# Kernel optimization log

Measured on AMD Instinct MI355X. Metric: run time of the kernel, lower is better.

Reference implementation:

```python
import jax, jax.numpy as jnp
import numpy as np

NUM_HEADS = 4
HEAD_DIM = 64
BN_EPS = 1e-5


def setup_inputs() -> dict:
    key = jax.random.key(0)
    ks = jax.random.split(key, 6)
    B, C, H, W = 8, 256, 48, 48
    HD = NUM_HEADS * HEAD_DIM  # 256
    x = jax.random.normal(ks[0], (B, C, H, W), dtype=jnp.float32)
    q_w = jax.random.normal(ks[1], (HD, C), dtype=jnp.float32) * (1.0 / np.sqrt(C))
    k_w = jax.random.normal(ks[2], (HEAD_DIM, C), dtype=jnp.float32) * (1.0 / np.sqrt(C))
    v_w = jax.random.normal(ks[3], (HEAD_DIM, C), dtype=jnp.float32) * (1.0 / np.sqrt(C))
    proj_w = jax.random.normal(ks[4], (C, HD), dtype=jnp.float32) * (1.0 / np.sqrt(HD))
    proj_b = jnp.zeros((C,), dtype=jnp.float32)
    gamma = jnp.ones((C,), dtype=jnp.float32)
    beta = jnp.zeros((C,), dtype=jnp.float32)
    return {"x": x, "q_w": q_w, "k_w": k_w, "v_w": v_w,
            "proj_w": proj_w, "proj_b": proj_b, "gamma": gamma, "beta": beta}


def reference(x, q_w, k_w, v_w, proj_w, proj_b, gamma, beta):
    B, C, H, W = x.shape
    N = H * W
    scale = HEAD_DIM ** -0.5
    xf = x.reshape(B, C, N)  # 1x1 conv == channel matmul
    q = jnp.einsum('oc,bcn->bon', q_w, xf).reshape(B, NUM_HEADS, HEAD_DIM, N)
    k = jnp.einsum('dc,bcn->bdn', k_w, xf)  # shared single KV head (MQA)
    v = jnp.einsum('dc,bcn->bdn', v_w, xf)
    # scores: [B, heads, N, N]
    attn = jnp.einsum('bhdn,bdm->bhnm', q, k) * scale
    attn = jax.nn.softmax(attn, axis=-1)
    out = jnp.einsum('bhnm,bdm->bhdn', attn, v)  # [B, heads, d, N]
    out = out.reshape(B, NUM_HEADS * HEAD_DIM, N)
    out = jnp.einsum('co,bon->bcn', proj_w, out) + proj_b[None, :, None]
    out = out.reshape(B, C, H, W)
    # BatchNorm2d (training-mode batch statistics, biased variance)
    mean = jnp.mean(out, axis=(0, 2, 3), keepdims=True)
    var = jnp.var(out, axis=(0, 2, 3), keepdims=True)
    out = gamma[None, :, None, None] * (out - mean) * jax.lax.rsqrt(var + BN_EPS) + beta[None, :, None, None]
    return out + x
```

## Files before the change

kernel.cpp:

```cpp
#include <hip/hip_runtime.h>
#include <hip/hip_bf16.h>
#include <math.h>

#define BB 8
#define CCH 256
#define NN 2304
#define NH 4
#define HDIM 64
#define QKV_ROWS 384
#define BN_EPS 1e-5f
#define NTILES 36
#define HTILES 18
#define SLOG2E 0.18033688011112042f

typedef short bf16x8 __attribute__((ext_vector_type(8)));
typedef short bf16x4 __attribute__((ext_vector_type(4)));
typedef float f32x4 __attribute__((ext_vector_type(4)));

#if __has_builtin(__builtin_amdgcn_exp2f)
#define EXP2(x) __builtin_amdgcn_exp2f(x)
#else
#define EXP2(x) __expf((x) * 0.6931471805599453f)
#endif

#define MFMA16(a, b, c) __builtin_amdgcn_mfma_f32_16x16x16bf16_1k(a, b, c, 0, 0, 0)
#define MFMA32(a, b, c) __builtin_amdgcn_mfma_f32_16x16x32_bf16(a, b, c, 0, 0, 0)

__device__ __forceinline__ unsigned bfpair(float a, float b) {
    __hip_bfloat162 h = __float22bfloat162_rn(make_float2(a, b));
    return *(unsigned*)&h;
}
__device__ __forceinline__ unsigned short f2bf(float f) {
    unsigned u = __float_as_uint(f);
    u = (u + 0x7FFFu + ((u >> 16) & 1u)) >> 16;
    return (unsigned short)u;
}
__device__ __forceinline__ bf16x4 pack4(float p0, float p1, float p2, float p3) {
    union { unsigned u[2]; bf16x4 v; } x;
    x.u[0] = bfpair(p0, p1);
    x.u[1] = bfpair(p2, p3);
    return x.v;
}
__device__ __forceinline__ float bf2f(unsigned short s) {
    return __uint_as_float((unsigned)s << 16);
}

__global__ __launch_bounds__(256) void cvt_x_k(
    const float* __restrict__ x, unsigned short* __restrict__ xT)
{
    __shared__ float sX[64][65];
    const int tid = threadIdx.x;
    const int b  = blockIdx.x;
    const int nb = blockIdx.y * 64;
    const int cb = blockIdx.z * 64;

    #pragma unroll
    for (int u = 0; u < 4; ++u) {
        int c  = (tid >> 4) + 16 * u;
        int n4 = (tid & 15) * 4;
        float4 v = *(const float4*)(x + ((size_t)(b * CCH + cb + c)) * NN + nb + n4);
        sX[c][n4+0] = v.x; sX[c][n4+1] = v.y; sX[c][n4+2] = v.z; sX[c][n4+3] = v.w;
    }
    __syncthreads();

    const int n  = tid >> 2;
    const int cg = (tid & 3) * 16;
    unsigned vals[8];
    #pragma unroll
    for (int p = 0; p < 8; ++p)
        vals[p] = bfpair(sX[cg + 2*p][n], sX[cg + 2*p + 1][n]);
    unsigned short* dst = xT + ((size_t)(b * NN + nb + n)) * CCH + cb + cg;
    *(uint4*)dst = make_uint4(vals[0], vals[1], vals[2], vals[3]);
    *(uint4*)(dst + 8) = make_uint4(vals[4], vals[5], vals[6], vals[7]);
}

__global__ __launch_bounds__(256) void cvt_w_k(
    const float* __restrict__ qw, const float* __restrict__ kw,
    const float* __restrict__ vw, const float* __restrict__ pw,
    unsigned short* __restrict__ Wb, unsigned short* __restrict__ Pb)
{
    int idx = blockIdx.x * 256 + threadIdx.x;
    if (idx < 98304) {
        int o = idx >> 8, c = idx & 255;
        float v;
        if (o < 256)      v = qw[(size_t)o * CCH + c] * SLOG2E;
        else if (o < 320) v = kw[(size_t)(o - 256) * CCH + c];
        else              v = vw[(size_t)(o - 320) * CCH + c];
        Wb[idx] = f2bf(v);
    } else {
        int j = idx - 98304;
        if (j < 65536) Pb[j] = f2bf(pw[j]);
    }
}

__global__ __launch_bounds__(128) void qkv_mfma_k(
    const unsigned short* __restrict__ Wb, const unsigned short* __restrict__ xT,
    unsigned short* __restrict__ Qt, unsigned short* __restrict__ Kt,
    unsigned short* __restrict__ Vn)
{
    __shared__ unsigned short sE[2][64 * 72];
    const int tid = threadIdx.x;
    const int wave = tid >> 6;
    const int lane = tid & 63;
    const int quad = lane >> 4;
    const int l15  = lane & 15;
    const int b  = blockIdx.x;
    const int nb = blockIdx.y * 64;
    const int mb = blockIdx.z * 128 + wave * 64;

    const unsigned short* Ab = Wb + (size_t)(mb + l15) * CCH + quad * 8;
    const unsigned short* Bb = xT + ((size_t)(b * NN + nb + l15)) * CCH + quad * 8;

    f32x4 C[4][4] = {};
    for (int k0 = 0; k0 < CCH; k0 += 32) {
        bf16x8 aA[4], bB[4];
        #pragma unroll
        for (int i = 0; i < 4; ++i) aA[i] = *(const bf16x8*)(Ab + (size_t)(16*i) * CCH + k0);
        #pragma unroll
        for (int j = 0; j < 4; ++j) bB[j] = *(const bf16x8*)(Bb + (size_t)(16*j) * CCH + k0);
        #pragma unroll
        for (int i = 0; i < 4; ++i)
            #pragma unroll
            for (int j = 0; j < 4; ++j)
                C[i][j] = MFMA32(aA[i], bB[j], C[i][j]);
    }

    unsigned short* sEw = &sE[wave][0];
    if (mb < 320) {
        #pragma unroll
        for (int i = 0; i < 4; ++i)
            #pragma unroll
            for (int j = 0; j < 4; ++j) {
                unsigned p01 = bfpair(C[i][j][0], C[i][j][1]);
                unsigned p23 = bfpair(C[i][j][2], C[i][j][3]);
                unsigned short* p = sEw + (16*j + l15) * 72 + 16*i + quad*4;
                *(unsigned*)p = p01;
                *(unsigned*)(p + 2) = p23;
            }
        if (mb < 256) {
            #pragma unroll
            for (int it = 0; it < 8; ++it) {
                int flat = lane + 64 * it;
                int row = flat >> 3;
                int o8  = (flat & 7) * 8;
                uint4 v = *(const uint4*)(sEw + row * 72 + o8);
                *(uint4*)(Qt + ((size_t)(b * NN + nb + row)) * CCH + mb + o8) = v;
            }
        } else {
            #pragma unroll
            for (int it = 0; it < 8; ++it) {
                int flat = lane + 64 * it;
                int row = flat >> 3;
                int o8  = (flat & 7) * 8;
                uint4 v = *(const uint4*)(sEw + row * 72 + o8);
                *(uint4*)(Kt + ((size_t)(b * NN + nb + row)) * 64 + o8) = v;
            }
        }
    } else {
        #pragma unroll
        for (int i = 0; i < 4; ++i)
            #pragma unroll
            for (int j = 0; j < 4; ++j) {
                unsigned p01 = bfpair(C[i][j][0], C[i][j][1]);
                unsigned p23 = bfpair(C[i][j][2], C[i][j][3]);
                unsigned short* p = sEw + (16*i + quad*4) * 72 + 16*j + l15;
                p[0]   = (unsigned short)p01;
                p[72]  = (unsigned short)(p01 >> 16);
                p[144] = (unsigned short)p23;
                p[216] = (unsigned short)(p23 >> 16);
            }
        #pragma unroll
        for (int it = 0; it < 8; ++it) {
            int flat = lane + 64 * it;
            int row = flat >> 3;
            int n8  = (flat & 7) * 8;
            uint4 v = *(const uint4*)(sEw + row * 72 + n8);
            *(uint4*)(Vn + ((size_t)(b * 64 + (mb - 320) + row)) * NN + nb + n8) = v;
        }
    }
}

__global__ __launch_bounds__(256, 4) void attn_k(
    const unsigned short* __restrict__ Qt,
    const unsigned short* __restrict__ Kt,
    const unsigned short* __restrict__ Vn,
    unsigned short* __restrict__ Ao)
{
    __shared__ __align__(16) unsigned short sKV[4 * 64 * 72];

    const int tid   = threadIdx.x;
    const int wave  = tid >> 6;
    const int lane  = tid & 63;
    const int quad  = lane >> 4;
    const int l15   = lane & 15;
    const int qslot = wave & 1;
    const int kh    = wave >> 1;
    const int qoff  = qslot * 32;
    const int b     = blockIdx.x;
    const int nb    = blockIdx.y * 64;
    const int head  = blockIdx.z;

    unsigned short* sKb = sKV + kh * 2 * 4608;
    unsigned short* sVb = sKb + 4608;

    bf16x8 bQ[2][2];
    const unsigned short* QtB = Qt + ((size_t)(b * NN + nb + qoff + l15)) * CCH + head * 64 + quad * 8;
    #pragma unroll
    for (int qt = 0; qt < 2; ++qt)
        #pragma unroll
        for (int s = 0; s < 2; ++s)
            bQ[qt][s] = *(const bf16x8*)(QtB + (size_t)(16*qt) * CCH + s * 32);

    bf16x8 pf[8];
    #pragma unroll
    for (int u = 0; u < 8; ++u) {
        const int buf   = u >> 1;
        const int khb   = buf >> 1;
        const int local = (u & 1) * 256 + tid;
        const int row   = local >> 3;
        const int ch8   = (local & 7) * 8;
        const int keys0 = khb * HTILES * 64;
        if ((buf & 1) == 0)
            pf[u] = *(const bf16x8*)(Kt + ((size_t)(b * NN + keys0 + row)) * 64 + ch8);
        else
            pf[u] = *(const bf16x8*)(Vn + ((size_t)(b * 64 + row)) * NN + keys0 + ch8);
    }

    f32x4 O[4][2] = {};
    float lacc[2] = {0.f, 0.f};

    for (int step = 0; step < HTILES; ++step) {
        __syncthreads();
        #pragma unroll
        for (int u = 0; u < 8; ++u) {
            const int buf   = u >> 1;
            const int local = (u & 1) * 256 + tid;
            const int row   = local >> 3;
            const int ch8   = (local & 7) * 8;
            *(bf16x8*)(sKV + buf * 4608 + row * 72 + ch8) = pf[u];
        }
        __syncthreads();

        if (step + 1 < HTILES) {
            #pragma unroll
            for (int u = 0; u < 8; ++u) {
                const int buf   = u >> 1;
                const int khb   = buf >> 1;
                const int local = (u & 1) * 256 + tid;
                const int row   = local >> 3;
                const int ch8   = (local & 7) * 8;
                const int keys0 = (khb * HTILES + step + 1) * 64;
                if ((buf & 1) == 0)
                    pf[u] = *(const bf16x8*)(Kt + ((size_t)(b * NN + keys0 + row)) * 64 + ch8);
                else
                    pf[u] = *(const bf16x8*)(Vn + ((size_t)(b * 64 + row)) * NN + keys0 + ch8);
            }
        }

        f32x4 C[4][2] = {};
        #pragma unroll
        for (int s = 0; s < 2; ++s)
            #pragma unroll
            for (int kt = 0; kt < 4; ++kt) {
                bf16x8 aK = *(const bf16x8*)(sKb + (16*kt + l15) * 72 + s * 32 + quad * 8);
                C[kt][0] = MFMA32(aK, bQ[0][s], C[kt][0]);
                C[kt][1] = MFMA32(aK, bQ[1][s], C[kt][1]);
            }

        bf16x4 bP[4][2];
        #pragma unroll
        for (int kt = 0; kt < 4; ++kt)
            #pragma unroll
            for (int qt = 0; qt < 2; ++qt) {
                float p0 = EXP2(C[kt][qt][0]);
                float p1 = EXP2(C[kt][qt][1]);
                float p2 = EXP2(C[kt][qt][2]);
                float p3 = EXP2(C[kt][qt][3]);
                lacc[qt] += (p0 + p1) + (p2 + p3);
                bP[kt][qt] = pack4(p0, p1, p2, p3);
            }

        #pragma unroll
        for (int jd = 0; jd < 4; ++jd)
            #pragma unroll
            for (int kt = 0; kt < 4; ++kt) {
                bf16x4 aV = *(const bf16x4*)(sVb + (16*jd + l15) * 72 + 16*kt + quad*4);
                O[jd][0] = MFMA16(aV, bP[kt][0], O[jd][0]);
                O[jd][1] = MFMA16(aV, bP[kt][1], O[jd][1]);
            }
    }
    __syncthreads();

    float* sc = (float*)sKV;
    unsigned short* sT = (unsigned short*)sKV + 9216;
    if (kh == 1) {
        const int base = qslot * 2304 + lane * 36;
        #pragma unroll
        for (int jd = 0; jd < 4; ++jd)
            #pragma unroll
            for (int qt = 0; qt < 2; ++qt)
                *(f32x4*)(sc + base + jd * 8 + qt * 4) = O[jd][qt];
        sc[base + 32] = lacc[0];
        sc[base + 33] = lacc[1];
    }
    __syncthreads();
    if (kh == 0) {
        const int base = qslot * 2304 + lane * 36;
        #pragma unroll
        for (int jd = 0; jd < 4; ++jd)
            #pragma unroll
            for (int qt = 0; qt < 2; ++qt)
                O[jd][qt] += *(const f32x4*)(sc + base + jd * 8 + qt * 4);
        lacc[0] += sc[base + 32];
        lacc[1] += sc[base + 33];

        float rinv[2];
        #pragma unroll
        for (int qt = 0; qt < 2; ++qt) {
            float s = lacc[qt];
            s += __shfl_xor(s, 16);
            s += __shfl_xor(s, 32);
            rinv[qt] = 1.0f / s;
        }
        #pragma unroll
        for (int qt = 0; qt < 2; ++qt)
            #pragma unroll
            for (int jd = 0; jd < 4; ++jd) {
                unsigned lo = bfpair(O[jd][qt][0] * rinv[qt], O[jd][qt][1] * rinv[qt]);
                unsigned hi = bfpair(O[jd][qt][2] * rinv[qt], O[jd][qt][3] * rinv[qt]);
                *(uint2*)(sT + (qoff + 16*qt + l15) * 72 + 16*jd + quad*4) = make_uint2(lo, hi);
            }
    }
    __syncthreads();

    #pragma unroll
    for (int it = 0; it < 2; ++it) {
        int flat = tid + 256 * it;
        int row = flat >> 3;
        int c8  = (flat & 7) * 8;
        uint4 v = *(const uint4*)(sT + row * 72 + c8);
        *(uint4*)(Ao + ((size_t)(b * NN + nb + row)) * CCH + head * 64 + c8) = v;
    }
}

__global__ __launch_bounds__(128) void proj_mfma_k(
    const unsigned short* __restrict__ Pb, const unsigned short* __restrict__ Ao,
    const float* __restrict__ pb, unsigned short* __restrict__ projb)
{
    __shared__ unsigned short sE[2][64 * 72];
    const int tid = threadIdx.x;
    const int wave = tid >> 6;
    const int lane = tid & 63;
    const int quad = lane >> 4;
    const int l15  = lane & 15;
    const int b  = blockIdx.x;
    const int nb = blockIdx.y * 64;
    const int mb = blockIdx.z * 128 + wave * 64;

    const unsigned short* Ab = Pb + (size_t)(mb + l15) * CCH + quad * 8;
    const unsigned short* Bb = Ao + ((size_t)(b * NN + nb + l15)) * CCH + quad * 8;

    f32x4 C[4][4] = {};
    for (int k0 = 0; k0 < CCH; k0 += 32) {
        bf16x8 aA[4], bB[4];
        #pragma unroll
        for (int i = 0; i < 4; ++i) aA[i] = *(const bf16x8*)(Ab + (size_t)(16*i) * CCH + k0);
        #pragma unroll
        for (int j = 0; j < 4; ++j) bB[j] = *(const bf16x8*)(Bb + (size_t)(16*j) * CCH + k0);
        #pragma unroll
        for (int i = 0; i < 4; ++i)
            #pragma unroll
            for (int j = 0; j < 4; ++j)
                C[i][j] = MFMA32(aA[i], bB[j], C[i][j]);
    }

    unsigned short* sEw = &sE[wave][0];
    #pragma unroll
    for (int i = 0; i < 4; ++i)
        #pragma unroll
        for (int j = 0; j < 4; ++j) {
            const float b0 = pb[mb + 16*i + quad*4 + 0];
            const float b1 = pb[mb + 16*i + quad*4 + 1];
            const float b2 = pb[mb + 16*i + quad*4 + 2];
            const float b3 = pb[mb + 16*i + quad*4 + 3];
            unsigned p01 = bfpair(C[i][j][0] + b0, C[i][j][1] + b1);
            unsigned p23 = bfpair(C[i][j][2] + b2, C[i][j][3] + b3);
            unsigned short* p = sEw + (16*i + quad*4) * 72 + 16*j + l15;
            p[0]   = (unsigned short)p01;
            p[72]  = (unsigned short)(p01 >> 16);
            p[144] = (unsigned short)p23;
            p[216] = (unsigned short)(p23 >> 16);
        }
    #pragma unroll
    for (int it = 0; it < 8; ++it) {
        int flat = lane + 64 * it;
        int row = flat >> 3;
        int n8  = (flat & 7) * 8;
        uint4 v = *(const uint4*)(sEw + row * 72 + n8);
        *(uint4*)(projb + ((size_t)(b * CCH + mb + row)) * NN + nb + n8) = v;
    }
}

__global__ __launch_bounds__(256) void bn_stats_k(
    const unsigned short* __restrict__ projb, const float* __restrict__ gamma,
    const float* __restrict__ beta, float* __restrict__ stats)
{
    const int c = blockIdx.x;
    const int tid = threadIdx.x;
    float s = 0.f, s2 = 0.f;
    for (int b = 0; b < BB; ++b) {
        const unsigned short* p = projb + ((size_t)(b * CCH + c)) * NN;
        for (int ch = tid; ch < NN / 8; ch += 256) {
            uint4 v = *(const uint4*)(p + ch * 8);
            const unsigned short* e = (const unsigned short*)&v;
            #pragma unroll
            for (int k = 0; k < 8; ++k) {
                float f = bf2f(e[k]);
                s += f; s2 += f * f;
            }
        }
    }
    __shared__ float rs[256], rs2[256];
    rs[tid] = s; rs2[tid] = s2;
    __syncthreads();
    for (int off = 128; off > 0; off >>= 1) {
        if (tid < off) { rs[tid] += rs[tid + off]; rs2[tid] += rs2[tid + off]; }
        __syncthreads();
    }
    if (tid == 0) {
        const float inv_n = 1.0f / (float)(BB * NN);
        float mean = rs[0] * inv_n;
        float var  = rs2[0] * inv_n - mean * mean;
        float sc = gamma[c] * rsqrtf(var + BN_EPS);
        stats[c] = sc;
        stats[CCH + c] = beta[c] - mean * sc;
    }
}

__global__ __launch_bounds__(256) void bn_apply_k(
    const unsigned short* __restrict__ projb, const float* __restrict__ x,
    const float* __restrict__ stats, float* __restrict__ out)
{
    size_t idx = ((size_t)blockIdx.x * 256 + threadIdx.x) * 8;
    const size_t total = (size_t)BB * CCH * NN;
    if (idx >= total) return;
    int c = (int)((idx / NN) % CCH);
    float sc = stats[c], sh = stats[CCH + c];
    uint4 pv = *(const uint4*)(projb + idx);
    const unsigned short* ps = (const unsigned short*)&pv;
    float4 x0 = *(const float4*)(x + idx);
    float4 x1 = *(const float4*)(x + idx + 4);
    float4 r0, r1;
    r0.x = sc * bf2f(ps[0]) + sh + x0.x;
    r0.y = sc * bf2f(ps[1]) + sh + x0.y;
    r0.z = sc * bf2f(ps[2]) + sh + x0.z;
    r0.w = sc * bf2f(ps[3]) + sh + x0.w;
    r1.x = sc * bf2f(ps[4]) + sh + x1.x;
    r1.y = sc * bf2f(ps[5]) + sh + x1.y;
    r1.z = sc * bf2f(ps[6]) + sh + x1.z;
    r1.w = sc * bf2f(ps[7]) + sh + x1.w;
    *(float4*)(out + idx) = r0;
    *(float4*)(out + idx + 4) = r1;
}

extern "C" void kernel_launch(void* const* d_in, const int* in_sizes, int n_in,
                              void* d_out, int out_size, void* d_ws, size_t ws_size,
                              hipStream_t stream)
{
    const float* x     = (const float*)d_in[0];
    const float* qw    = (const float*)d_in[1];
    const float* kw    = (const float*)d_in[2];
    const float* vw    = (const float*)d_in[3];
    const float* pw    = (const float*)d_in[4];
    const float* pb    = (const float*)d_in[5];
    const float* gamma = (const float*)d_in[6];
    const float* beta  = (const float*)d_in[7];
    float* out = (float*)d_out;

    char* ws = (char*)d_ws;
    unsigned short* xT = (unsigned short*)ws;
    unsigned short* Ao = (unsigned short*)ws;
    unsigned short* Wb = (unsigned short*)(ws + 9437184);
    unsigned short* Pb = (unsigned short*)(ws + 9633792);
    unsigned short* Qt = (unsigned short*)(ws + 9764864);
    unsigned short* Kt = (unsigned short*)(ws + 19202048);
    unsigned short* Vn = (unsigned short*)(ws + 21561344);
    unsigned short* projb = (unsigned short*)(ws + 9764864);
    float* stats = (float*)(ws + 28639232);

    cvt_w_k<<<640, 256, 0, stream>>>(qw, kw, vw, pw, Wb, Pb);

    dim3 g0(BB, NN / 64, CCH / 64);
    cvt_x_k<<<g0, 256, 0, stream>>>(x, xT);

    dim3 g1(BB, NN / 64, 3);
    qkv_mfma_k<<<g1, 128, 0, stream>>>(Wb, xT, Qt, Kt, Vn);

    dim3 g2(BB, NN / 64, NH);
    attn_k<<<g2, 256, 0, stream>>>(Qt, Kt, Vn, Ao);

    dim3 g3(BB, NN / 64, 2);
    proj_mfma_k<<<g3, 128, 0, stream>>>(Pb, Ao, pb, projb);

    bn_stats_k<<<CCH, 256, 0, stream>>>(projb, gamma, beta, stats);

    int total8 = BB * CCH * NN / 8;
    bn_apply_k<<<(total8 + 255) / 256, 256, 0, stream>>>(projb, x, stats, out);
}
```

Before: 202.0 us.

## Swizzle attention LDS tiles, raise occupancy, and double-buffer GEMM register loads

The attention kernel's K/V shared-memory tiles drop the 72-element padded stride for a 64-element stride with an XOR swizzle on 16-byte chunks. This shrinks LDS per block while still avoiding bank conflicts, and launch bounds are raised from 4 to 5 blocks per SM. The QKV and projection GEMM kernels now fully unroll the K loop and prefetch the next k-slice into a second register buffer, so global loads overlap the MFMAs. The cost is more VGPR pressure, and the higher occupancy target may force register spills in attn_k.

```diff
diff --git a/kernel.cpp b/kernel.cpp
--- a/kernel.cpp
+++ b/kernel.cpp
@@ -112,17 +112,27 @@
     const unsigned short* Bb = xT + ((size_t)(b * NN + nb + l15)) * CCH + quad * 8;
 
     f32x4 C[4][4] = {};
-    for (int k0 = 0; k0 < CCH; k0 += 32) {
-        bf16x8 aA[4], bB[4];
-        #pragma unroll
-        for (int i = 0; i < 4; ++i) aA[i] = *(const bf16x8*)(Ab + (size_t)(16*i) * CCH + k0);
-        #pragma unroll
-        for (int j = 0; j < 4; ++j) bB[j] = *(const bf16x8*)(Bb + (size_t)(16*j) * CCH + k0);
+    bf16x8 aA[2][4], bB[2][4];
+    #pragma unroll
+    for (int i = 0; i < 4; ++i) aA[0][i] = *(const bf16x8*)(Ab + (size_t)(16*i) * CCH);
+    #pragma unroll
+    for (int j = 0; j < 4; ++j) bB[0][j] = *(const bf16x8*)(Bb + (size_t)(16*j) * CCH);
+
+    #pragma unroll
+    for (int kk = 0; kk < 8; ++kk) {
+        const int cur = kk & 1;
+        if (kk < 7) {
+            const int k1 = (kk + 1) * 32;
+            #pragma unroll
+            for (int i = 0; i < 4; ++i) aA[cur^1][i] = *(const bf16x8*)(Ab + (size_t)(16*i) * CCH + k1);
+            #pragma unroll
+            for (int j = 0; j < 4; ++j) bB[cur^1][j] = *(const bf16x8*)(Bb + (size_t)(16*j) * CCH + k1);
+        }
         #pragma unroll
         for (int i = 0; i < 4; ++i)
             #pragma unroll
             for (int j = 0; j < 4; ++j)
-                C[i][j] = MFMA32(aA[i], bB[j], C[i][j]);
+                C[i][j] = MFMA32(aA[cur][i], bB[cur][j], C[i][j]);
     }
 
     unsigned short* sEw = &sE[wave][0];
@@ -180,13 +190,13 @@
     }
 }
 
-__global__ __launch_bounds__(256, 4) void attn_k(
+__global__ __launch_bounds__(256, 5) void attn_k(
     const unsigned short* __restrict__ Qt,
     const unsigned short* __restrict__ Kt,
     const unsigned short* __restrict__ Vn,
     unsigned short* __restrict__ Ao)
 {
-    __shared__ __align__(16) unsigned short sKV[4 * 64 * 72];
+    __shared__ __align__(16) unsigned short sKV[4 * 64 * 64];
 
     const int tid   = threadIdx.x;
     const int wave  = tid >> 6;
@@ -200,8 +210,8 @@
     const int nb    = blockIdx.y * 64;
     const int head  = blockIdx.z;
 
-    unsigned short* sKb = sKV + kh * 2 * 4608;
-    unsigned short* sVb = sKb + 4608;
+    unsigned short* sKb = sKV + kh * 2 * 4096;
+    unsigned short* sVb = sKb + 4096;
 
     bf16x8 bQ[2][2];
     const unsigned short* QtB = Qt + ((size_t)(b * NN + nb + qoff + l15)) * CCH + head * 64 + quad * 8;
@@ -236,8 +246,8 @@
             const int buf   = u >> 1;
             const int local = (u & 1) * 256 + tid;
             const int row   = local >> 3;
-            const int ch8   = (local & 7) * 8;
-            *(bf16x8*)(sKV + buf * 4608 + row * 72 + ch8) = pf[u];
+            const int chsw  = ((local & 7) ^ (row & 7)) * 8;
+            *(bf16x8*)(sKV + buf * 4096 + row * 64 + chsw) = pf[u];
         }
         __syncthreads();
 
@@ -262,7 +272,9 @@
         for (int s = 0; s < 2; ++s)
             #pragma unroll
             for (int kt = 0; kt < 4; ++kt) {
-                bf16x8 aK = *(const bf16x8*)(sKb + (16*kt + l15) * 72 + s * 32 + quad * 8);
+                const int row = 16*kt + l15;
+                const int chsw = ((s*4 + quad) ^ (row & 7)) * 8;
+                bf16x8 aK = *(const bf16x8*)(sKb + row * 64 + chsw);
                 C[kt][0] = MFMA32(aK, bQ[0][s], C[kt][0]);
                 C[kt][1] = MFMA32(aK, bQ[1][s], C[kt][1]);
             }
@@ -284,7 +296,9 @@
         for (int jd = 0; jd < 4; ++jd)
             #pragma unroll
             for (int kt = 0; kt < 4; ++kt) {
-                bf16x4 aV = *(const bf16x4*)(sVb + (16*jd + l15) * 72 + 16*kt + quad*4);
+                const int row = 16*jd + l15;
+                const int chsw = ((2*kt + (quad >> 1)) ^ (row & 7)) * 8 + (quad & 1) * 4;
+                bf16x4 aV = *(const bf16x4*)(sVb + row * 64 + chsw);
                 O[jd][0] = MFMA16(aV, bP[kt][0], O[jd][0]);
                 O[jd][1] = MFMA16(aV, bP[kt][1], O[jd][1]);
             }
@@ -361,17 +375,27 @@
     const unsigned short* Bb = Ao + ((size_t)(b * NN + nb + l15)) * CCH + quad * 8;
 
     f32x4 C[4][4] = {};
-    for (int k0 = 0; k0 < CCH; k0 += 32) {
-        bf16x8 aA[4], bB[4];
-        #pragma unroll
-        for (int i = 0; i < 4; ++i) aA[i] = *(const bf16x8*)(Ab + (size_t)(16*i) * CCH + k0);
-        #pragma unroll
-        for (int j = 0; j < 4; ++j) bB[j] = *(const bf16x8*)(Bb + (size_t)(16*j) * CCH + k0);
+    bf16x8 aA[2][4], bB[2][4];
+    #pragma unroll
+    for (int i = 0; i < 4; ++i) aA[0][i] = *(const bf16x8*)(Ab + (size_t)(16*i) * CCH);
+    #pragma unroll
+    for (int j = 0; j < 4; ++j) bB[0][j] = *(const bf16x8*)(Bb + (size_t)(16*j) * CCH);
+
+    #pragma unroll
+    for (int kk = 0; kk < 8; ++kk) {
+        const int cur = kk & 1;
+        if (kk < 7) {
+            const int k1 = (kk + 1) * 32;
+            #pragma unroll
+            for (int i = 0; i < 4; ++i) aA[cur^1][i] = *(const bf16x8*)(Ab + (size_t)(16*i) * CCH + k1);
+            #pragma unroll
+            for (int j = 0; j < 4; ++j) bB[cur^1][j] = *(const bf16x8*)(Bb + (size_t)(16*j) * CCH + k1);
+        }
         #pragma unroll
         for (int i = 0; i < 4; ++i)
             #pragma unroll
             for (int j = 0; j < 4; ++j)
-                C[i][j] = MFMA32(aA[i], bB[j], C[i][j]);
+                C[i][j] = MFMA32(aA[cur][i], bB[cur][j], C[i][j]);
     }
 
     unsigned short* sEw = &sE[wave][0];
```

Measured after the change: 237.2 us. 1.17x slower.
